# Optimization experiments

Measured on AMD Instinct MI355X. Metric: run time of the kernel, lower is better.

## Reference

```python
import jax, jax.numpy as jnp
import numpy as np

B, N, M, U = 8, 4096, 2048, 4096
IMG = 640.0
NUM_CLASSES = 81  # COCO-like, class 0 = person


def _make_boxes(key, shape2d):
    """Valid xyxy boxes: x2>x1, y2>y1, inside a IMGxIMG canvas."""
    k1, k2 = jax.random.split(key)
    xy = jax.random.uniform(k1, shape2d + (2,), dtype=jnp.float32) * (IMG * 0.8)
    wh = jax.random.uniform(k2, shape2d + (2,), dtype=jnp.float32) * (IMG * 0.2) + 1.0
    return jnp.concatenate([xy, xy + wh], axis=-1)


def setup_inputs() -> dict:
    key = jax.random.key(0)
    ks = jax.random.split(key, 8)
    pred_boxes = _make_boxes(ks[0], (B, N))
    gt_boxes = _make_boxes(ks[1], (B, M))
    gt_valid = jax.random.uniform(ks[2], (B, M)) < 0.9
    gt_boxes = jnp.where(gt_valid[..., None], gt_boxes, 0.0)
    pred_scores = jax.random.uniform(ks[3], (B, N), dtype=jnp.float32)
    pred_classes = jax.random.randint(ks[4], (B, N), 0, NUM_CLASSES, dtype=jnp.int32)
    union_scores = jax.random.uniform(ks[5], (U,), dtype=jnp.float32)
    union_classes = jax.random.randint(ks[6], (U,), 0, NUM_CLASSES, dtype=jnp.int32)
    return {
        "pred_boxes": pred_boxes,
        "pred_scores": pred_scores,
        "pred_classes": pred_classes,
        "gt_boxes": gt_boxes,
        "union_scores": union_scores,
        "union_classes": union_classes,
    }


def reference(pred_boxes, pred_scores, pred_classes, gt_boxes, union_scores, union_classes):
    # --- fused pairwise IoU, replacing the per-box python loop ---
    p = pred_boxes[:, :, None, :]   # [B, N, 1, 4]
    g = gt_boxes[:, None, :, :]     # [B, 1, M, 4]
    iw = jnp.maximum(jnp.minimum(p[..., 2], g[..., 2]) - jnp.maximum(p[..., 0], g[..., 0]), 0.0)
    ih = jnp.maximum(jnp.minimum(p[..., 3], g[..., 3]) - jnp.maximum(p[..., 1], g[..., 1]), 0.0)
    inters = iw * ih                # [B, N, M]
    area_p = (p[..., 2] - p[..., 0]) * (p[..., 3] - p[..., 1])
    area_g = (g[..., 2] - g[..., 0]) * (g[..., 3] - g[..., 1])
    uni = area_p + area_g - inters
    iou = inters / jnp.maximum(uni, 1e-9)

    # preds filtered to people class (==0); gt rows with zero sum filtered out
    pred_is_person = pred_classes == 0                       # [B, N]
    gt_valid = jnp.sum(gt_boxes, axis=-1) != 0               # [B, M]
    pair_mask = pred_is_person[:, :, None] & gt_valid[:, None, :]
    iou = jnp.where(pair_mask, iou, 0.0)

    iou_max = jnp.max(iou, axis=(1, 2))                      # [B]
    # max_iou_t[i] set only when people_scores non-empty
    has_person = jnp.any(pred_is_person, axis=1)
    iou_max = jnp.where(has_person, iou_max, 0.0)
    max_iou_t = jnp.mean(iou_max)

    # union-image detection: max score among person detections
    max_prob_t = jnp.max(jnp.where(union_classes == 0, union_scores, -jnp.inf))

    return jnp.stack([max_prob_t, max_iou_t])
```

## Files before the change

### kernel.cpp

```cpp
#include <hip/hip_runtime.h>
#include <math.h>

#define BATCH  8
#define NPRED  4096
#define MGT    2048
#define UU     4096
#define SPB    8
#define NSLOT  (BATCH * SPB)
#define PSLICE (NPRED / SPB)
#define GPT    (MGT / 256)
#define MAGIC  0xC0FFEE00u
#define SLOT_STRIDE 16

__global__ __launch_bounds__(256) void fused_kernel(
    const float4* __restrict__ pred_boxes,
    const int2*   __restrict__ pred_classes2,
    const float4* __restrict__ gt_boxes,
    const float4* __restrict__ union_scores4,
    const int4*   __restrict__ union_classes4,
    unsigned long long* __restrict__ slots,
    float* __restrict__ out)
{
    const int tid = threadIdx.x;
    const int blk = blockIdx.x;

    if (blk < NSLOT) {
        __shared__ float4 plist[PSLICE];
        __shared__ float  parea[PSLICE];
        __shared__ int    lcount;
        __shared__ float  wmax[4];

        const int b    = blk >> 3;
        const int psub = blk & 7;

        const int  cbase = b * (NPRED / 2) + psub * (PSLICE / 2) + tid;
        const int2 cl    = pred_classes2[cbase];
        const int  pb    = cbase * 2;
        const float4 bx0 = pred_boxes[pb + 0];
        const float4 bx1 = pred_boxes[pb + 1];

        float4 g[GPT];
        #pragma unroll
        for (int k = 0; k < GPT; ++k)
            g[k] = gt_boxes[b * MGT + k * 256 + tid];

        float ga[GPT];
        #pragma unroll
        for (int k = 0; k < GPT; ++k)
            ga[k] = (g[k].z - g[k].x) * (g[k].w - g[k].y);

        if (tid == 0) lcount = 0;
        __syncthreads();

        if (cl.x == 0) { int p = atomicAdd(&lcount, 1); plist[p] = bx0; parea[p] = (bx0.z - bx0.x) * (bx0.w - bx0.y); }
        if (cl.y == 0) { int p = atomicAdd(&lcount, 1); plist[p] = bx1; parea[p] = (bx1.z - bx1.x) * (bx1.w - bx1.y); }
        __syncthreads();

        const int cnt = lcount;
        float best[GPT];
        #pragma unroll
        for (int k = 0; k < GPT; ++k) best[k] = 0.0f;

        for (int j = 0; j < cnt; ++j) {
            const float4 p  = plist[j];
            const float  ap = parea[j];
            #pragma unroll
            for (int k = 0; k < GPT; ++k) {
                float iw = fminf(p.z, g[k].z) - fmaxf(p.x, g[k].x);
                float ih = fminf(p.w, g[k].w) - fmaxf(p.y, g[k].y);
                iw = fmaxf(iw, 0.0f); ih = fmaxf(ih, 0.0f);
                const float inter = iw * ih;
                const float uni   = ap + ga[k] - inter;
                best[k] = fmaxf(best[k], inter * __builtin_amdgcn_rcpf(fmaxf(uni, 1e-9f)));
            }
        }

        float bestv = best[0];
        #pragma unroll
        for (int k = 1; k < GPT; ++k) bestv = fmaxf(bestv, best[k]);

        #pragma unroll
        for (int off = 32; off >= 1; off >>= 1)
            bestv = fmaxf(bestv, __shfl_xor(bestv, off));
        if ((tid & 63) == 0) wmax[tid >> 6] = bestv;
        __syncthreads();
        if (tid == 0) {
            const float m = fmaxf(fmaxf(wmax[0], wmax[1]), fmaxf(wmax[2], wmax[3]));
            const unsigned long long v =
                ((unsigned long long)MAGIC << 32) | (unsigned long long)__float_as_uint(m);
            __hip_atomic_store(&slots[blk * SLOT_STRIDE], v,
                               __ATOMIC_RELAXED, __HIP_MEMORY_SCOPE_AGENT);
        }
    } else {
        __shared__ float pmax[4];
        float mp = -INFINITY;
        #pragma unroll
        for (int s = 0; s < UU / (256 * 4); ++s) {
            const int i = s * 256 + tid;
            const int4   c = union_classes4[i];
            const float4 v = union_scores4[i];
            if (c.x == 0) mp = fmaxf(mp, v.x);
            if (c.y == 0) mp = fmaxf(mp, v.y);
            if (c.z == 0) mp = fmaxf(mp, v.z);
            if (c.w == 0) mp = fmaxf(mp, v.w);
        }
        #pragma unroll
        for (int off = 32; off >= 1; off >>= 1)
            mp = fmaxf(mp, __shfl_xor(mp, off));
        if ((tid & 63) == 0) pmax[tid >> 6] = mp;
        __syncthreads();
        if (tid == 0)
            out[0] = fmaxf(fmaxf(pmax[0], pmax[1]), fmaxf(pmax[2], pmax[3]));

        if (tid < 64) {
            unsigned long long v;
            do {
                v = __hip_atomic_load(&slots[tid * SLOT_STRIDE],
                                      __ATOMIC_RELAXED, __HIP_MEMORY_SCOPE_AGENT);
            } while ((unsigned int)(v >> 32) != MAGIC);
            __hip_atomic_store(&slots[tid * SLOT_STRIDE], 0ULL,
                               __ATOMIC_RELAXED, __HIP_MEMORY_SCOPE_AGENT);

            unsigned int q = (unsigned int)v;
            q = max(q, (unsigned int)__shfl_xor((int)q, 1, 8));
            q = max(q, (unsigned int)__shfl_xor((int)q, 2, 8));
            q = max(q, (unsigned int)__shfl_xor((int)q, 4, 8));
            float s = 0.0f;
            #pragma unroll
            for (int i = 0; i < 8; ++i)
                s += __uint_as_float((unsigned int)__shfl((int)q, 8 * i, 64));
            if (tid == 0)
                out[1] = s * 0.125f;
        }
    }
}

extern "C" void kernel_launch(void* const* d_in, const int* in_sizes, int n_in,
                              void* d_out, int out_size, void* d_ws, size_t ws_size,
                              hipStream_t stream) {
    const float4* pred_boxes    = (const float4*)d_in[0];
    const int2*   pred_classes2 = (const int2*)d_in[2];
    const float4* gt_boxes      = (const float4*)d_in[3];
    const float4* union_scores4 = (const float4*)d_in[4];
    const int4*   union_classes4= (const int4*)d_in[5];
    float* out = (float*)d_out;
    unsigned long long* slots = (unsigned long long*)d_ws;

    fused_kernel<<<NSLOT + 1, 256, 0, stream>>>(pred_boxes, pred_classes2, gt_boxes,
                                                union_scores4, union_classes4, slots, out);
}
```

Before: 14.20 us.

## Replace spin-waiting consumer block with last-arriver snapshot finalization

Every block, including the union-score block, now publishes a tagged result into its own workspace slot. After its stores complete, each block's first wave snapshots all slots. Whichever block sees every slot tagged writes both outputs and clears the slots. This removes the dedicated block that busy-polled the 64 producer slots, along with the dependence on that block being scheduled and spinning. In exchange, every block pays an extra read of all slots plus a wave vote, and correctness rests on relaxed agent-scope atomics and the vmcnt wait making each block's publish visible before it reads the others.

```diff
diff --git a/kernel.cpp b/kernel.cpp
--- a/kernel.cpp
+++ b/kernel.cpp
@@ -6,11 +6,51 @@
 #define MGT    2048
 #define UU     4096
 #define SPB    8
-#define NSLOT  (BATCH * SPB)
+#define NPROD  (BATCH * SPB)
 #define PSLICE (NPRED / SPB)
 #define GPT    (MGT / 256)
 #define MAGIC  0xC0FFEE00u
-#define SLOT_STRIDE 16
+#define STRIDE 16
+
+__device__ __forceinline__ void snapshot_finalize(
+    unsigned long long* __restrict__ slots,
+    float* __restrict__ out,
+    int tid, int blk, unsigned long long myv)
+{
+    asm volatile("s_waitcnt vmcnt(0)" ::: "memory");
+
+    if (tid >= 64) return;
+    const int lane = tid;
+
+    unsigned long long v = (blk == lane)
+        ? myv
+        : __hip_atomic_load(&slots[lane * STRIDE], __ATOMIC_RELAXED, __HIP_MEMORY_SCOPE_AGENT);
+    unsigned long long vu = myv;
+    if (blk != NPROD && lane == 0)
+        vu = __hip_atomic_load(&slots[NPROD * STRIDE], __ATOMIC_RELAXED, __HIP_MEMORY_SCOPE_AGENT);
+
+    const int ok64 = __all((unsigned int)(v >> 32) == MAGIC);
+    const int okU  = __shfl((int)((unsigned int)(vu >> 32) == MAGIC), 0);
+    if (!(ok64 && okU)) return;
+
+    const unsigned int ubits = (unsigned int)__shfl((int)(unsigned int)vu, 0);
+
+    unsigned int q = (unsigned int)v;
+    q = max(q, (unsigned int)__shfl_xor((int)q, 1, 8));
+    q = max(q, (unsigned int)__shfl_xor((int)q, 2, 8));
+    q = max(q, (unsigned int)__shfl_xor((int)q, 4, 8));
+    float s = 0.0f;
+    #pragma unroll
+    for (int i = 0; i < 8; ++i)
+        s += __uint_as_float((unsigned int)__shfl((int)q, 8 * i, 64));
+
+    if (lane == 0) {
+        out[0] = __uint_as_float(ubits);
+        out[1] = s * 0.125f;
+        __hip_atomic_store(&slots[NPROD * STRIDE], 0ULL, __ATOMIC_RELAXED, __HIP_MEMORY_SCOPE_AGENT);
+    }
+    __hip_atomic_store(&slots[lane * STRIDE], 0ULL, __ATOMIC_RELAXED, __HIP_MEMORY_SCOPE_AGENT);
+}
 
 __global__ __launch_bounds__(256) void fused_kernel(
     const float4* __restrict__ pred_boxes,
@@ -24,20 +64,22 @@
     const int tid = threadIdx.x;
     const int blk = blockIdx.x;
 
-    if (blk < NSLOT) {
+    __shared__ float red[4];
+
+    unsigned long long myv;
+
+    if (blk < NPROD) {
         __shared__ float4 plist[PSLICE];
         __shared__ float  parea[PSLICE];
         __shared__ int    lcount;
-        __shared__ float  wmax[4];
 
         const int b    = blk >> 3;
         const int psub = blk & 7;
 
         const int  cbase = b * (NPRED / 2) + psub * (PSLICE / 2) + tid;
         const int2 cl    = pred_classes2[cbase];
-        const int  pb    = cbase * 2;
-        const float4 bx0 = pred_boxes[pb + 0];
-        const float4 bx1 = pred_boxes[pb + 1];
+        const float4 bx0 = pred_boxes[cbase * 2 + 0];
+        const float4 bx1 = pred_boxes[cbase * 2 + 1];
 
         float4 g[GPT];
         #pragma unroll
@@ -82,17 +124,15 @@
         #pragma unroll
         for (int off = 32; off >= 1; off >>= 1)
             bestv = fmaxf(bestv, __shfl_xor(bestv, off));
-        if ((tid & 63) == 0) wmax[tid >> 6] = bestv;
+        if ((tid & 63) == 0) red[tid >> 6] = bestv;
         __syncthreads();
-        if (tid == 0) {
-            const float m = fmaxf(fmaxf(wmax[0], wmax[1]), fmaxf(wmax[2], wmax[3]));
-            const unsigned long long v =
-                ((unsigned long long)MAGIC << 32) | (unsigned long long)__float_as_uint(m);
-            __hip_atomic_store(&slots[blk * SLOT_STRIDE], v,
+
+        const float m = fmaxf(fmaxf(red[0], red[1]), fmaxf(red[2], red[3]));
+        myv = ((unsigned long long)MAGIC << 32) | (unsigned long long)__float_as_uint(m);
+        if (tid == 0)
+            __hip_atomic_store(&slots[blk * STRIDE], myv,
                                __ATOMIC_RELAXED, __HIP_MEMORY_SCOPE_AGENT);
-        }
     } else {
-        __shared__ float pmax[4];
         float mp = -INFINITY;
         #pragma unroll
         for (int s = 0; s < UU / (256 * 4); ++s) {
@@ -107,32 +147,17 @@
         #pragma unroll
         for (int off = 32; off >= 1; off >>= 1)
             mp = fmaxf(mp, __shfl_xor(mp, off));
-        if ((tid & 63) == 0) pmax[tid >> 6] = mp;
+        if ((tid & 63) == 0) red[tid >> 6] = mp;
         __syncthreads();
+
+        const float m = fmaxf(fmaxf(red[0], red[1]), fmaxf(red[2], red[3]));
+        myv = ((unsigned long long)MAGIC << 32) | (unsigned long long)__float_as_uint(m);
         if (tid == 0)
-            out[0] = fmaxf(fmaxf(pmax[0], pmax[1]), fmaxf(pmax[2], pmax[3]));
+            __hip_atomic_store(&slots[NPROD * STRIDE], myv,
+                               __ATOMIC_RELAXED, __HIP_MEMORY_SCOPE_AGENT);
+    }
 
-        if (tid < 64) {
-            unsigned long long v;
-            do {
-                v = __hip_atomic_load(&slots[tid * SLOT_STRIDE],
-                                      __ATOMIC_RELAXED, __HIP_MEMORY_SCOPE_AGENT);
-            } while ((unsigned int)(v >> 32) != MAGIC);
-            __hip_atomic_store(&slots[tid * SLOT_STRIDE], 0ULL,
-                               __ATOMIC_RELAXED, __HIP_MEMORY_SCOPE_AGENT);
-
-            unsigned int q = (unsigned int)v;
-            q = max(q, (unsigned int)__shfl_xor((int)q, 1, 8));
-            q = max(q, (unsigned int)__shfl_xor((int)q, 2, 8));
-            q = max(q, (unsigned int)__shfl_xor((int)q, 4, 8));
-            float s = 0.0f;
-            #pragma unroll
-            for (int i = 0; i < 8; ++i)
-                s += __uint_as_float((unsigned int)__shfl((int)q, 8 * i, 64));
-            if (tid == 0)
-                out[1] = s * 0.125f;
-        }
-    }
+    snapshot_finalize(slots, out, tid, blk, myv);
 }
 
 extern "C" void kernel_launch(void* const* d_in, const int* in_sizes, int n_in,
@@ -146,6 +171,6 @@
     float* out = (float*)d_out;
     unsigned long long* slots = (unsigned long long*)d_ws;
 
-    fused_kernel<<<NSLOT + 1, 256, 0, stream>>>(pred_boxes, pred_classes2, gt_boxes,
+    fused_kernel<<<NPROD + 1, 256, 0, stream>>>(pred_boxes, pred_classes2, gt_boxes,
                                                 union_scores4, union_classes4, slots, out);
 }
```

Measured after the change: 12.30 us. -13.4%, faster.
